# Kernel tuning notes

Measured on AMD Instinct MI355X. Metric: run time of the kernel, lower is better.

## Reference

```python
import jax, jax.numpy as jnp
import numpy as np

NU, NI, NR = 50000, 50000, 5   # users, items, rating levels
D, B, LS, LI = 64, 512, 32, 64 # embed_dim, batch, max social nbrs, max item hist
NEG = -1e9


def setup_inputs() -> dict:
    key = jax.random.key(0)
    ks = iter(jax.random.split(key, 64))
    def lin(din, dout):
        s = 1.0 / np.sqrt(din)
        return (jax.random.uniform(next(ks), (din, dout), minval=-s, maxval=s, dtype=jnp.float32),
                jax.random.uniform(next(ks), (dout,), minval=-s, maxval=s, dtype=jnp.float32))
    inp = {}
    inp['user_w'] = jax.random.normal(next(ks), (NU, D), dtype=jnp.float32) * 0.1
    inp['item_w'] = jax.random.normal(next(ks), (NI, D), dtype=jnp.float32) * 0.1
    inp['rating_w'] = jax.random.normal(next(ks), (NR, D), dtype=jnp.float32) * 0.1
    for name, din, dout in [('i_ln1', 2*D, D), ('i_ln2', D, D), ('i_ln3', 2*D, D),
                            ('i_att1', 2*D, D), ('i_att2', D, D), ('i_att3', D, 1),
                            ('s_ln1', D, D), ('s_ln2', 2*D, D), ('s_ln3', D, D),
                            ('s_att1', 2*D, D), ('s_att2', D, D), ('s_att3', D, 1)]:
        w, b = lin(din, dout)
        inp[name + '_w'] = w
        inp[name + '_b'] = b
    inp['nodes'] = jax.random.randint(next(ks), (B,), 0, NU)
    inp['social_hist'] = jax.random.randint(next(ks), (NU, LS), 0, NU)
    inp['social_mask'] = jax.random.bernoulli(next(ks), 0.5, (NU, LS)).at[:, 0].set(True)
    inp['item_hist'] = jax.random.randint(next(ks), (NU, LI), 0, NI)
    inp['rating_hist'] = jax.random.randint(next(ks), (NU, LI), 0, NR)
    inp['item_mask'] = jax.random.bernoulli(next(ks), 0.5, (NU, LI)).at[:, 0].set(True)
    return inp


def reference(user_w, item_w, rating_w,
              i_ln1_w, i_ln1_b, i_ln2_w, i_ln2_b, i_ln3_w, i_ln3_b,
              i_att1_w, i_att1_b, i_att2_w, i_att2_b, i_att3_w, i_att3_b,
              s_ln1_w, s_ln1_b, s_ln2_w, s_ln2_b, s_ln3_w, s_ln3_b,
              s_att1_w, s_att1_b, s_att2_w, s_att2_b, s_att3_w, s_att3_b,
              nodes, social_hist, social_mask, item_hist, rating_hist, item_mask):
    relu = jax.nn.relu

    def attn(x, w1, b1, w2, b2, w3, b3, mask):
        # x: [..., L, 2D] -> softmax weights over valid neighbors: [..., L]
        h = relu(x @ w1 + b1)
        h = relu(h @ w2 + b2)
        logit = (h @ w3 + b3)[..., 0]
        logit = jnp.where(mask, logit, NEG)
        return jax.nn.softmax(logit, axis=-1)

    def item_final(uids):
        # uids: any shape [...]; returns [..., D]  (Aggre_item.item_final)
        its, rts, m = item_hist[uids], rating_hist[uids], item_mask[uids]
        x = jnp.concatenate([item_w[its], rating_w[rts]], axis=-1)   # [...,LI,2D]
        x = relu(x @ i_ln1_w + i_ln1_b)                              # [...,LI,D]
        u = user_w[uids]                                             # [...,D]
        a_in = jnp.concatenate([x, jnp.broadcast_to(u[..., None, :], x.shape)], axis=-1)
        alpha = attn(a_in, i_att1_w, i_att1_b, i_att2_w, i_att2_b, i_att3_w, i_att3_b, m)
        hI = jnp.einsum('...l,...ld->...d', alpha, x)                # attention-weighted sum
        hI = relu(hI @ i_ln2_w + i_ln2_b)
        return relu(jnp.concatenate([u, hI], axis=-1) @ i_ln3_w + i_ln3_b)

    # item-space factor of query users
    hI_self = item_final(nodes)                                      # [B,D]
    # social aggregation: item_final over each user's social neighbors
    nbrs, nmask = social_hist[nodes], social_mask[nodes]             # [B,LS]
    hI_nb = item_final(nbrs)                                         # [B,LS,D]
    u = user_w[nodes]                                                # [B,D]
    b_in = jnp.concatenate([hI_nb, jnp.broadcast_to(u[:, None, :], hI_nb.shape)], axis=-1)
    beta = attn(b_in, s_att1_w, s_att1_b, s_att2_w, s_att2_b, s_att3_w, s_att3_b, nmask)
    hS = jnp.einsum('bl,bld->bd', beta, hI_nb)
    hS = relu(hS @ s_ln1_w + s_ln1_b)
    f = jnp.concatenate([hI_self, hS], axis=-1)
    f = relu(f @ s_ln2_w + s_ln2_b)
    return relu(f @ s_ln3_w + s_ln3_b)
```

## Files before the change

kernel.cpp:

```cpp
#include <hip/hip_runtime.h>
#include <math.h>


#define NII 50000
#define BB 512
#define LSS 32
#define NT 16896

typedef short short8 __attribute__((ext_vector_type(8)));
typedef float f32x4 __attribute__((ext_vector_type(4)));

static __device__ __forceinline__ bool mread(const void* p, long i, int mode) {
  if (mode == 0) return ((const int*)p)[i] != 0;
  if (mode == 2) return ((const float*)p)[i] != 0.0f;
  return ((const unsigned char*)p)[i] != 0;
}

static __device__ __forceinline__ float wsum(float v) {
#pragma unroll
  for (int s = 1; s < 64; s <<= 1) v += __shfl_xor(v, s);
  return v;
}
static __device__ __forceinline__ float wmax(float v) {
#pragma unroll
  for (int s = 1; s < 64; s <<= 1) v = fmaxf(v, __shfl_xor(v, s));
  return v;
}
static __device__ __forceinline__ float rsum16(float v) {
#pragma unroll
  for (int s = 1; s < 16; s <<= 1) v += __shfl_xor(v, s);
  return v;
}

static __device__ __forceinline__ short bf16rne(float f) {
  unsigned u = __float_as_uint(f);
  u = (u + 0x7FFFu + ((u >> 16) & 1u)) >> 16;
  return (short)u;
}
static __device__ __forceinline__ float bf16tof(short h) {
  return __uint_as_float(((unsigned)(unsigned short)h) << 16);
}

static __device__ __forceinline__ void wave_fence() {
  asm volatile("s_waitcnt lgkmcnt(0)" ::: "memory");
  __builtin_amdgcn_sched_barrier(0);
}

static __device__ __forceinline__ bool inst_uid(int t, const int* nodes,
                                                const int* social_hist,
                                                const void* social_mask,
                                                int mode, long* uid) {
  if (t < BB) {
    *uid = nodes[t];
    return true;
  }
  const int nb = t - BB;
  const int b = nb >> 5, l = nb & 31;
  const long mi = (long)nodes[b] * LSS + l;
  if (!mread(social_mask, mi, mode)) return false;
  *uid = social_hist[mi];
  return true;
}

__global__ void setup_kernel(const unsigned int* __restrict__ sm,
                             int* __restrict__ flag,
                             const float* __restrict__ rating_w,
                             const float* __restrict__ w1,
                             const float* __restrict__ b1,
                             float* __restrict__ RW1g,
                             const float* __restrict__ A1w,
                             const float* __restrict__ A2w,
                             short* __restrict__ B1,
                             short* __restrict__ B2,
                             short* __restrict__ W1hi,
                             short* __restrict__ W1lo) {
  const int tid = threadIdx.x;
  if (blockIdx.x == 0) {
    __shared__ int notInt, notFloat;
    if (tid == 0) { notInt = 0; notFloat = 0; }
    __syncthreads();
    int ni = 0, nf = 0;
    for (int i = tid; i < 4096; i += 256) {
      unsigned int x = sm[i];
      if (x > 1u) ni = 1;
      if (x != 0u && x != 0x3F800000u) nf = 1;
    }
    if (ni) atomicOr(&notInt, 1);
    if (nf) atomicOr(&notFloat, 1);
    __syncthreads();
    if (tid == 0) flag[0] = notInt ? (notFloat ? 1 : 2) : 0;
  } else if (blockIdx.x == 1) {
    for (int t = tid; t < 320; t += 256) {
      const int r = t >> 6, c = t & 63;
      float acc = b1[c];
      for (int k = 0; k < 64; ++k)
        acc = fmaf(rating_w[r * 64 + k], w1[(64 + k) * 64 + c], acc);
      RW1g[r * 64 + c] = acc;
    }
  } else {
    for (int idx = tid; idx < 4096; idx += 256) {
      int e = idx & 7, g = idx >> 3;
      int l = g & 63, q = g >> 6;
      int kb = q >> 2, nb = q & 3;
      int k = kb * 32 + ((l >> 4) & 3) * 8 + e;
      int col = nb * 16 + (l & 15);
      B1[idx] = bf16rne(A1w[k * 64 + col]);
      B2[idx] = bf16rne(A2w[k * 64 + col]);
      float a = w1[k * 64 + col];
      short h = bf16rne(a);
      W1hi[idx] = h;
      W1lo[idx] = bf16rne(a - bf16tof(h));
    }
  }
}

__global__ __launch_bounds__(256, 2)
void mid_kernel(const float* __restrict__ item_w,
                const short* __restrict__ W1hi,
                const short* __restrict__ W1lo,
                short* __restrict__ xbase16,
                const float* __restrict__ user_w,
                const float* __restrict__ A1w, const float* __restrict__ A1b,
                const int* __restrict__ nodes,
                const int* __restrict__ social_hist,
                float* __restrict__ uA1buf) {
  const int tid = threadIdx.x, lane = tid & 63, w = tid >> 6;
  if (blockIdx.x < 512) {
    const int l15 = lane & 15, lg4 = lane >> 4;
    short8 bh[8], bl[8];
#pragma unroll
    for (int q = 0; q < 8; ++q) {
      bh[q] = *(const short8*)(W1hi + (q * 64 + lane) * 8);
      bl[q] = *(const short8*)(W1lo + (q * 64 + lane) * 8);
    }
    const int wid = blockIdx.x * 4 + w;
    for (int tile = wid; tile < 3125; tile += 2048) {
      const long r0 = (long)tile * 16;
      const float* ap = item_w + (r0 + l15) * 64 + lg4 * 8;
      short8 ah[2], al[2];
#pragma unroll
      for (int kb = 0; kb < 2; ++kb) {
        const float4 a = *(const float4*)(ap + kb * 32);
        const float4 b = *(const float4*)(ap + kb * 32 + 4);
        float v[8] = {a.x, a.y, a.z, a.w, b.x, b.y, b.z, b.w};
        short8 hi, lo;
#pragma unroll
        for (int e = 0; e < 8; ++e) {
          short h = bf16rne(v[e]);
          hi[e] = h;
          lo[e] = bf16rne(v[e] - bf16tof(h));
        }
        ah[kb] = hi;
        al[kb] = lo;
      }
#pragma unroll
      for (int nb = 0; nb < 4; ++nb) {
        f32x4 acc = {0.0f, 0.0f, 0.0f, 0.0f};
        acc = __builtin_amdgcn_mfma_f32_16x16x32_bf16(ah[0], bh[0 * 4 + nb], acc, 0, 0, 0);
        acc = __builtin_amdgcn_mfma_f32_16x16x32_bf16(ah[1], bh[1 * 4 + nb], acc, 0, 0, 0);
        acc = __builtin_amdgcn_mfma_f32_16x16x32_bf16(ah[0], bl[0 * 4 + nb], acc, 0, 0, 0);
        acc = __builtin_amdgcn_mfma_f32_16x16x32_bf16(ah[1], bl[1 * 4 + nb], acc, 0, 0, 0);
        acc = __builtin_amdgcn_mfma_f32_16x16x32_bf16(al[0], bh[0 * 4 + nb], acc, 0, 0, 0);
        acc = __builtin_amdgcn_mfma_f32_16x16x32_bf16(al[1], bh[1 * 4 + nb], acc, 0, 0, 0);
#pragma unroll
        for (int r = 0; r < 4; ++r)
          xbase16[(r0 + lg4 * 4 + r) * 64 + nb * 16 + l15] = bf16rne(acc[r]);
      }
    }
  } else {
    const int i0 = (blockIdx.x - 512) * 64;
    __shared__ float sW[64][64], sU[64][64];
    __shared__ float sb[64];
    __shared__ int sUid[64];
    for (int i = tid; i < 4096; i += 256) sW[i >> 6][i & 63] = A1w[4096 + i];
    if (tid < 64) {
      sb[tid] = A1b[tid];
      const int t = i0 + tid;
      int uid;
      if (t < BB) {
        uid = nodes[t];
      } else {
        const int nb = t - BB;
        uid = social_hist[(long)nodes[nb >> 5] * LSS + (nb & 31)];
      }
      sUid[tid] = uid;
    }
    __syncthreads();
    for (int i = tid; i < 4096; i += 256) {
      int r = i >> 6, c = i & 63;
      sU[r][c] = user_w[(long)sUid[r] * 64 + c];
    }
    __syncthreads();
    float acc[16];
#pragma unroll
    for (int r = 0; r < 16; ++r) acc[r] = sb[lane];
    for (int k = 0; k < 64; k += 4) {
      float wv0 = sW[k][lane], wv1 = sW[k + 1][lane];
      float wv2 = sW[k + 2][lane], wv3 = sW[k + 3][lane];
#pragma unroll
      for (int r = 0; r < 16; ++r) {
        const float4 xv = *(const float4*)(&sU[w * 16 + r][k]);
        acc[r] = fmaf(xv.x, wv0, acc[r]);
        acc[r] = fmaf(xv.y, wv1, acc[r]);
        acc[r] = fmaf(xv.z, wv2, acc[r]);
        acc[r] = fmaf(xv.w, wv3, acc[r]);
      }
    }
#pragma unroll
    for (int r = 0; r < 16; ++r)
      uA1buf[(long)(i0 + w * 16 + r) * 64 + lane] = acc[r];
  }
}

__global__ __launch_bounds__(512, 8)
void core_mfma_kernel(const short* __restrict__ xb16,
                      const float* __restrict__ RW1g,
                      const float* __restrict__ uA1buf,
                      const short* __restrict__ Bimg1,
                      const short* __restrict__ Bimg2,
                      const float* __restrict__ A2b,
                      const float* __restrict__ A3w,
                      const int* __restrict__ item_hist,
                      const int* __restrict__ rating_hist,
                      const void* __restrict__ item_mask,
                      const int* __restrict__ flagp,
                      const int* __restrict__ nodes,
                      const int* __restrict__ social_hist,
                      const void* __restrict__ social_mask,
                      float* __restrict__ hvecbuf) {
  __shared__ __align__(16) short sB1[4096], sB2[4096];
  __shared__ __align__(16) char smem[8][3072];
  const int tid = threadIdx.x, lane = tid & 63, w = tid >> 6;

  short* h1w = (short*)(smem[w]);
  float* lgw = (float*)(smem[w] + 2304);
  int* cw = (int*)(smem[w] + 2560);

  ((int4*)sB1)[tid] = ((const int4*)Bimg1)[tid];
  ((int4*)sB2)[tid] = ((const int4*)Bimg2)[tid];
  __syncthreads();

  const int t = blockIdx.x * 8 + w;
  const int mode = flagp[0];
  long uid;
  if (!inst_uid(t, nodes, social_hist, social_mask, mode, &uid))
    return;

  const float a2bv = A2b[lane];
  const float a3v = A3w[lane];
  const int l15 = lane & 15;
  const int lg4 = lane >> 4;

#define B1F(q) (*(const short8*)(sB1 + ((q) * 64 + lane) * 8))
#define B2F(q) (*(const short8*)(sB2 + ((q) * 64 + lane) * 8))

  const long mbase = uid * 64;
  bool mk = mread(item_mask, mbase + lane, mode);
  unsigned long long bal = __ballot(mk);
  const int nact = (int)__popcll(bal);
  int pos = (int)__popcll(bal & ((1ull << lane) - 1ull));
  if (mk) cw[pos] = (item_hist[mbase + lane] << 3) | rating_hist[mbase + lane];
  const float uA1v = uA1buf[(long)t * 64 + lane];
  wave_fence();

  const int ng = (nact + 15) >> 4;
  for (int mc = 0; mc < ng; ++mc) {
    wave_fence();
    int row = mc * 16 + l15;
    if (row >= nact) row = nact - 1;
    const int p = cw[row];
    const long it = p >> 3;
    const int rt = p & 7;
    short8 xa[2];
#pragma unroll
    for (int kb = 0; kb < 2; ++kb) {
      const int koff = kb * 32 + lg4 * 8;
      const short8 xb = *(const short8*)(xb16 + it * 64 + koff);
      const float* rp = RW1g + rt * 64 + koff;
      const float4 c = *(const float4*)rp;
      const float4 d = *(const float4*)(rp + 4);
      short8 f;
      f[0] = bf16rne(fmaxf(bf16tof(xb[0]) + c.x, 0.0f));
      f[1] = bf16rne(fmaxf(bf16tof(xb[1]) + c.y, 0.0f));
      f[2] = bf16rne(fmaxf(bf16tof(xb[2]) + c.z, 0.0f));
      f[3] = bf16rne(fmaxf(bf16tof(xb[3]) + c.w, 0.0f));
      f[4] = bf16rne(fmaxf(bf16tof(xb[4]) + d.x, 0.0f));
      f[5] = bf16rne(fmaxf(bf16tof(xb[5]) + d.y, 0.0f));
      f[6] = bf16rne(fmaxf(bf16tof(xb[6]) + d.z, 0.0f));
      f[7] = bf16rne(fmaxf(bf16tof(xb[7]) + d.w, 0.0f));
      xa[kb] = f;
    }
#pragma unroll
    for (int nb = 0; nb < 4; ++nb) {
      const float ui = __shfl(uA1v, nb * 16 + l15);
      f32x4 acc = {ui, ui, ui, ui};
      acc = __builtin_amdgcn_mfma_f32_16x16x32_bf16(xa[0], B1F(0 * 4 + nb), acc, 0, 0, 0);
      acc = __builtin_amdgcn_mfma_f32_16x16x32_bf16(xa[1], B1F(1 * 4 + nb), acc, 0, 0, 0);
#pragma unroll
      for (int r = 0; r < 4; ++r)
        h1w[(lg4 * 4 + r) * 72 + nb * 16 + l15] = bf16rne(fmaxf(acc[r], 0.0f));
    }
    wave_fence();
    short8 ha[2];
    ha[0] = *(const short8*)(h1w + l15 * 72 + lg4 * 8);
    ha[1] = *(const short8*)(h1w + l15 * 72 + 32 + lg4 * 8);
    float t0 = 0.0f, t1 = 0.0f, t2 = 0.0f, t3 = 0.0f;
#pragma unroll
    for (int nb = 0; nb < 4; ++nb) {
      const float b2 = __shfl(a2bv, nb * 16 + l15);
      f32x4 acc = {b2, b2, b2, b2};
      acc = __builtin_amdgcn_mfma_f32_16x16x32_bf16(ha[0], B2F(0 * 4 + nb), acc, 0, 0, 0);
      acc = __builtin_amdgcn_mfma_f32_16x16x32_bf16(ha[1], B2F(1 * 4 + nb), acc, 0, 0, 0);
      const float a3c = __shfl(a3v, nb * 16 + l15);
      t0 = fmaf(fmaxf(acc[0], 0.0f), a3c, t0);
      t1 = fmaf(fmaxf(acc[1], 0.0f), a3c, t1);
      t2 = fmaf(fmaxf(acc[2], 0.0f), a3c, t2);
      t3 = fmaf(fmaxf(acc[3], 0.0f), a3c, t3);
    }
    t0 = rsum16(t0); t1 = rsum16(t1); t2 = rsum16(t2); t3 = rsum16(t3);
    if (l15 == 0) {
      const int jb = mc * 16 + lg4 * 4;
      lgw[jb + 0] = t0;
      lgw[jb + 1] = t1;
      lgw[jb + 2] = t2;
      lgw[jb + 3] = t3;
    }
  }
  wave_fence();

  const bool valid = (lane < nact);
  float lv = valid ? lgw[lane] : -1e30f;
  float mx = wmax(lv);
  float e = valid ? __expf(lv - mx) : 0.0f;
  float s = wsum(e);
  const float alpha = e / s;

  float h0 = 0.0f, hA = 0.0f, hB = 0.0f, hC = 0.0f;
  int j = 0;
  for (; j + 3 < nact; j += 4) {
    const int p0 = cw[j], p1 = cw[j + 1], p2 = cw[j + 2], p3 = cw[j + 3];
    const float a0 = __shfl(alpha, j), a1 = __shfl(alpha, j + 1);
    const float a2 = __shfl(alpha, j + 2), a3 = __shfl(alpha, j + 3);
    const float x0 = bf16tof(xb16[(long)(p0 >> 3) * 64 + lane]) + RW1g[(p0 & 7) * 64 + lane];
    const float x1 = bf16tof(xb16[(long)(p1 >> 3) * 64 + lane]) + RW1g[(p1 & 7) * 64 + lane];
    const float x2 = bf16tof(xb16[(long)(p2 >> 3) * 64 + lane]) + RW1g[(p2 & 7) * 64 + lane];
    const float x3 = bf16tof(xb16[(long)(p3 >> 3) * 64 + lane]) + RW1g[(p3 & 7) * 64 + lane];
    h0 = fmaf(a0, fmaxf(x0, 0.0f), h0);
    hA = fmaf(a1, fmaxf(x1, 0.0f), hA);
    hB = fmaf(a2, fmaxf(x2, 0.0f), hB);
    hC = fmaf(a3, fmaxf(x3, 0.0f), hC);
  }
  for (; j < nact; ++j) {
    const int p = cw[j];
    const float aj = __shfl(alpha, j);
    const float xv = bf16tof(xb16[(long)(p >> 3) * 64 + lane]) + RW1g[(p & 7) * 64 + lane];
    h0 = fmaf(aj, fmaxf(xv, 0.0f), h0);
  }
  hvecbuf[(long)t * 64 + lane] = (h0 + hA) + (hB + hC);
#undef B1F
#undef B2F
}

__global__ __launch_bounds__(256, 2)
void hI2final_kernel(const float* __restrict__ hvecbuf,
                     const float* __restrict__ user_w,
                     const float* __restrict__ W2w, const float* __restrict__ W2b,
                     const float* __restrict__ W3w, const float* __restrict__ W3b,
                     const int* __restrict__ nodes,
                     const int* __restrict__ social_hist,
                     float* __restrict__ hIbuf) {
  const int tid = threadIdx.x, lane = tid & 63, w = tid >> 6;
  const int i0 = blockIdx.x * 32;
  __shared__ float sW[128][64];
  __shared__ float sX[32][128];
  __shared__ float sb[64];
  __shared__ int sUid[32];
  for (int i = tid; i < 4096; i += 256) sW[i >> 6][i & 63] = W2w[i];
  if (tid < 64) sb[tid] = W2b[tid];
  if (tid < 32) {
    const int t = i0 + tid;
    int uid;
    if (t < BB) {
      uid = nodes[t];
    } else {
      const int nb = t - BB;
      uid = social_hist[(long)nodes[nb >> 5] * LSS + (nb & 31)];
    }
    sUid[tid] = uid;
  }
  __syncthreads();
  for (int i = tid; i < 2048; i += 256) {
    int r = i >> 6, c = i & 63;
    sX[r][64 + c] = hvecbuf[(long)(i0 + r) * 64 + c];
    sX[r][c] = user_w[(long)sUid[r] * 64 + c];
  }
  __syncthreads();

  float acc[8];
  {
    const float bv = sb[lane];
#pragma unroll
    for (int r = 0; r < 8; ++r) acc[r] = bv;
    for (int k = 0; k < 64; k += 4) {
      float wv0 = sW[k][lane], wv1 = sW[k + 1][lane];
      float wv2 = sW[k + 2][lane], wv3 = sW[k + 3][lane];
#pragma unroll
      for (int r = 0; r < 8; ++r) {
        const float4 xv = *(const float4*)(&sX[w * 8 + r][64 + k]);
        acc[r] = fmaf(xv.x, wv0, acc[r]);
        acc[r] = fmaf(xv.y, wv1, acc[r]);
        acc[r] = fmaf(xv.z, wv2, acc[r]);
        acc[r] = fmaf(xv.w, wv3, acc[r]);
      }
    }
#pragma unroll
    for (int r = 0; r < 8; ++r) sX[w * 8 + r][64 + lane] = fmaxf(acc[r], 0.0f);
  }
  __syncthreads();
  for (int i = tid; i < 8192; i += 256) sW[i >> 6][i & 63] = W3w[i];
  if (tid < 64) sb[tid] = W3b[tid];
  __syncthreads();

  {
    const float bv = sb[lane];
#pragma unroll
    for (int r = 0; r < 8; ++r) acc[r] = bv;
    for (int k = 0; k < 128; k += 4) {
      float wv0 = sW[k][lane], wv1 = sW[k + 1][lane];
      float wv2 = sW[k + 2][lane], wv3 = sW[k + 3][lane];
#pragma unroll
      for (int r = 0; r < 8; ++r) {
        const float4 xv = *(const float4*)(&sX[w * 8 + r][k]);
        acc[r] = fmaf(xv.x, wv0, acc[r]);
        acc[r] = fmaf(xv.y, wv1, acc[r]);
        acc[r] = fmaf(xv.z, wv2, acc[r]);
        acc[r] = fmaf(xv.w, wv3, acc[r]);
      }
    }
#pragma unroll
    for (int r = 0; r < 8; ++r)
      hIbuf[(long)(i0 + w * 8 + r) * 64 + lane] = fmaxf(acc[r], 0.0f);
  }
}

__global__ __launch_bounds__(256, 8)
void social_fused_kernel(const float* __restrict__ hIbuf,
                         const float* __restrict__ user_w,
                         const float* __restrict__ S1w,
                         const float* __restrict__ S1b,
                         const float* __restrict__ S2w,
                         const float* __restrict__ S2b,
                         const float* __restrict__ S3w,
                         const float* __restrict__ L1w, const float* __restrict__ L1b,
                         const float* __restrict__ L2w, const float* __restrict__ L2b,
                         const float* __restrict__ L3w, const float* __restrict__ L3b,
                         const int* __restrict__ nodes,
                         const void* __restrict__ social_mask,
                         const int* __restrict__ flagp,
                         float* __restrict__ out) {
  __shared__ __align__(16) short sB1[4096], sB2[4096];
  __shared__ __align__(16) char smem[4][3584];
  const int tid = threadIdx.x, lane = tid & 63, w = tid >> 6;
  short* h1w = (short*)(smem[w]);
  float* lgw = (float*)(smem[w] + 2560);
  int* cw = (int*)(smem[w] + 2816);
  float* vA = (float*)(smem[w] + 3072);
  float* vB = (float*)(smem[w] + 3328);

  for (int i = tid; i < 4096; i += 256) {
    int e = i & 7, g = i >> 3;
    int l = g & 63, q = g >> 6;
    int kb = q >> 2, nb = q & 3;
    int k = kb * 32 + ((l >> 4) & 3) * 8 + e;
    int col = nb * 16 + (l & 15);
    sB1[i] = bf16rne(S1w[k * 64 + col]);
    sB2[i] = bf16rne(S2w[k * 64 + col]);
  }
  __syncthreads();

  const int mode = flagp[0];
  const int l15 = lane & 15;
  const int lg4 = lane >> 4;
  const int b = blockIdx.x * 4 + w;
  const long uid = nodes[b];

  bool m = (lane < LSS) ? mread(social_mask, uid * LSS + lane, mode) : false;
  unsigned long long bal = __ballot(m);
  const int nval = (int)__popcll(bal);
  int pos = (int)__popcll(bal & ((1ull << lane) - 1ull));
  if (m) cw[pos] = lane;

  const float uv = user_w[uid * 64 + lane];
  float uA1v = S1b[lane];
#pragma unroll 8
  for (int k = 0; k < 64; ++k)
    uA1v = fmaf(__shfl(uv, k), S1w[(64 + k) * 64 + lane], uA1v);
  const float a2bv = S2b[lane];
  const float a3v = S3w[lane];
  wave_fence();

  const long hbase = 512L + (long)b * 32;
  const int ng = (nval + 15) >> 4;
  for (int mc = 0; mc < ng; ++mc) {
    wave_fence();
    int row = mc * 16 + l15;
    if (row >= nval) row = nval - 1;
    const long hrow = hbase + cw[row];
    short8 xa[2];
#pragma unroll
    for (int kb = 0; kb < 2; ++kb) {
      const float* xp = hIbuf + hrow * 64 + kb * 32 + lg4 * 8;
      const float4 a = *(const float4*)xp;
      const float4 bb = *(const float4*)(xp + 4);
      short8 f;
      f[0] = bf16rne(a.x);  f[1] = bf16rne(a.y);
      f[2] = bf16rne(a.z);  f[3] = bf16rne(a.w);
      f[4] = bf16rne(bb.x); f[5] = bf16rne(bb.y);
      f[6] = bf16rne(bb.z); f[7] = bf16rne(bb.w);
      xa[kb] = f;
    }
#pragma unroll
    for (int nb = 0; nb < 4; ++nb) {
      const float ui = __shfl(uA1v, nb * 16 + l15);
      f32x4 acc = {ui, ui, ui, ui};
      acc = __builtin_amdgcn_mfma_f32_16x16x32_bf16(
          xa[0], *(const short8*)(sB1 + ((0 * 4 + nb) * 64 + lane) * 8), acc, 0, 0, 0);
      acc = __builtin_amdgcn_mfma_f32_16x16x32_bf16(
          xa[1], *(const short8*)(sB1 + ((1 * 4 + nb) * 64 + lane) * 8), acc, 0, 0, 0);
#pragma unroll
      for (int r = 0; r < 4; ++r)
        h1w[(lg4 * 4 + r) * 80 + nb * 16 + l15] = bf16rne(fmaxf(acc[r], 0.0f));
    }
    wave_fence();
    short8 ha[2];
    ha[0] = *(const short8*)(h1w + l15 * 80 + lg4 * 8);
    ha[1] = *(const short8*)(h1w + l15 * 80 + 32 + lg4 * 8);
    float t0 = 0.0f, t1 = 0.0f, t2 = 0.0f, t3 = 0.0f;
#pragma unroll
    for (int nb = 0; nb < 4; ++nb) {
      const float b2 = __shfl(a2bv, nb * 16 + l15);
      f32x4 acc = {b2, b2, b2, b2};
      acc = __builtin_amdgcn_mfma_f32_16x16x32_bf16(
          ha[0], *(const short8*)(sB2 + ((0 * 4 + nb) * 64 + lane) * 8), acc, 0, 0, 0);
      acc = __builtin_amdgcn_mfma_f32_16x16x32_bf16(
          ha[1], *(const short8*)(sB2 + ((1 * 4 + nb) * 64 + lane) * 8), acc, 0, 0, 0);
      const float a3c = __shfl(a3v, nb * 16 + l15);
      t0 = fmaf(fmaxf(acc[0], 0.0f), a3c, t0);
      t1 = fmaf(fmaxf(acc[1], 0.0f), a3c, t1);
      t2 = fmaf(fmaxf(acc[2], 0.0f), a3c, t2);
      t3 = fmaf(fmaxf(acc[3], 0.0f), a3c, t3);
    }
    t0 = rsum16(t0); t1 = rsum16(t1); t2 = rsum16(t2); t3 = rsum16(t3);
    if (l15 == 0) {
      const int jb = mc * 16 + lg4 * 4;
      lgw[jb + 0] = t0;
      lgw[jb + 1] = t1;
      lgw[jb + 2] = t2;
      lgw[jb + 3] = t3;
    }
  }
  wave_fence();

  const bool valid = (lane < nval);
  float lv = valid ? lgw[lane] : -1e30f;
  float mx = wmax(lv);
  float e = valid ? __expf(lv - mx) : 0.0f;
  float s = wsum(e);
  const float beta = e / s;

  float hs = 0.0f;
  for (int j = 0; j < nval; ++j) {
    const float bj = __shfl(beta, j);
    hs = fmaf(bj, hIbuf[(hbase + cw[j]) * 64 + lane], hs);
  }

  vA[lane] = hs;
  wave_fence();
  float acc = L1b[lane];
#pragma unroll 8
  for (int k = 0; k < 64; ++k) acc = fmaf(vA[k], L1w[k * 64 + lane], acc);
  const float vecB = fmaxf(acc, 0.0f);
  const float selfv = hIbuf[(long)b * 64 + lane];
  wave_fence();
  vA[lane] = selfv;
  vB[lane] = vecB;
  wave_fence();
  acc = L2b[lane];
#pragma unroll 8
  for (int k = 0; k < 64; ++k) acc = fmaf(vA[k], L2w[k * 64 + lane], acc);
#pragma unroll 8
  for (int k = 0; k < 64; ++k) acc = fmaf(vB[k], L2w[(64 + k) * 64 + lane], acc);
  const float fv = fmaxf(acc, 0.0f);
  wave_fence();
  vA[lane] = fv;
  wave_fence();
  acc = L3b[lane];
#pragma unroll 8
  for (int k = 0; k < 64; ++k) acc = fmaf(vA[k], L3w[k * 64 + lane], acc);
  out[(long)b * 64 + lane] = fmaxf(acc, 0.0f);
}

extern "C" void kernel_launch(void* const* d_in, const int* in_sizes, int n_in,
                              void* d_out, int out_size, void* d_ws, size_t ws_size,
                              hipStream_t stream) {
  const float* user_w   = (const float*)d_in[0];
  const float* item_w   = (const float*)d_in[1];
  const float* rating_w = (const float*)d_in[2];
  const float* i_ln1_w  = (const float*)d_in[3];
  const float* i_ln1_b  = (const float*)d_in[4];
  const float* i_ln2_w  = (const float*)d_in[5];
  const float* i_ln2_b  = (const float*)d_in[6];
  const float* i_ln3_w  = (const float*)d_in[7];
  const float* i_ln3_b  = (const float*)d_in[8];
  const float* i_att1_w = (const float*)d_in[9];
  const float* i_att1_b = (const float*)d_in[10];
  const float* i_att2_w = (const float*)d_in[11];
  const float* i_att2_b = (const float*)d_in[12];
  const float* i_att3_w = (const float*)d_in[13];
  const float* i_att3_b = (const float*)d_in[14];
  const float* s_ln1_w  = (const float*)d_in[15];
  const float* s_ln1_b  = (const float*)d_in[16];
  const float* s_ln2_w  = (const float*)d_in[17];
  const float* s_ln2_b  = (const float*)d_in[18];
  const float* s_ln3_w  = (const float*)d_in[19];
  const float* s_ln3_b  = (const float*)d_in[20];
  const float* s_att1_w = (const float*)d_in[21];
  const float* s_att1_b = (const float*)d_in[22];
  const float* s_att2_w = (const float*)d_in[23];
  const float* s_att2_b = (const float*)d_in[24];
  const float* s_att3_w = (const float*)d_in[25];
  const float* s_att3_b = (const float*)d_in[26];
  const int*  nodes       = (const int*)d_in[27];
  const int*  social_hist = (const int*)d_in[28];
  const void* social_mask = d_in[29];
  const int*  item_hist   = (const int*)d_in[30];
  const int*  rating_hist = (const int*)d_in[31];
  const void* item_mask   = d_in[32];

  char* ws = (char*)d_ws;
  int*   flag    = (int*)(ws + 0);
  float* uA1buf  = (float*)(ws + 135680);
  float* hIbuf   = uA1buf;
  float* hvecbuf = (float*)(ws + 4461056);
  short* W1hi    = (short*)(ws + 4461056);
  short* W1lo    = (short*)(ws + 4469248);
  short* xbase16 = (short*)(ws + 8786432);
  float* RW1g    = (float*)(ws + 21586432);
  short* Bimg1   = (short*)(ws + 21587712);
  short* Bimg2   = (short*)(ws + 21595904);

  setup_kernel<<<3, 256, 0, stream>>>(
      (const unsigned int*)social_mask, flag,
      rating_w, i_ln1_w, i_ln1_b, RW1g,
      i_att1_w, i_att2_w, Bimg1, Bimg2, W1hi, W1lo);
  mid_kernel<<<512 + NT / 64, 256, 0, stream>>>(
      item_w, W1hi, W1lo, xbase16,
      user_w, i_att1_w, i_att1_b, nodes, social_hist, uA1buf);
  core_mfma_kernel<<<NT / 8, 512, 0, stream>>>(
      xbase16, RW1g, uA1buf, Bimg1, Bimg2, i_att2_b, i_att3_w,
      item_hist, rating_hist, item_mask, flag,
      nodes, social_hist, social_mask, hvecbuf);
  hI2final_kernel<<<NT / 32, 256, 0, stream>>>(
      hvecbuf, user_w, i_ln2_w, i_ln2_b, i_ln3_w, i_ln3_b,
      nodes, social_hist, hIbuf);
  social_fused_kernel<<<BB / 4, 256, 0, stream>>>(
      hIbuf, user_w, s_att1_w, s_att1_b, s_att2_w, s_att2_b, s_att3_w,
      s_ln1_w, s_ln1_b, s_ln2_w, s_ln2_b, s_ln3_w, s_ln3_b,
      nodes, social_mask, flag, (float*)d_out);
}
```

Before: 107.6 us.

## Software-pipeline item-chunk gathers with double-buffered registers in attention MLP

The loop over 16-row item chunks is unrolled into four fixed stages. The global gather of the next chunk's bf16 item rows is issued before the MFMA work on the current chunk, so memory latency overlaps compute. s_setprio is raised around the MFMA sections to favour this wave's matrix issue. The unrolling assumes at most 64 active items (LI=64), and the extra live registers may reduce occupancy.

```diff
diff --git a/kernel.cpp b/kernel.cpp
--- a/kernel.cpp
+++ b/kernel.cpp
@@ -264,68 +264,94 @@
   wave_fence();
 
   const int ng = (nact + 15) >> 4;
-  for (int mc = 0; mc < ng; ++mc) {
-    wave_fence();
-    int row = mc * 16 + l15;
-    if (row >= nact) row = nact - 1;
-    const int p = cw[row];
-    const long it = p >> 3;
-    const int rt = p & 7;
-    short8 xa[2];
-#pragma unroll
-    for (int kb = 0; kb < 2; ++kb) {
-      const int koff = kb * 32 + lg4 * 8;
-      const short8 xb = *(const short8*)(xb16 + it * 64 + koff);
-      const float* rp = RW1g + rt * 64 + koff;
-      const float4 c = *(const float4*)rp;
-      const float4 d = *(const float4*)(rp + 4);
-      short8 f;
-      f[0] = bf16rne(fmaxf(bf16tof(xb[0]) + c.x, 0.0f));
-      f[1] = bf16rne(fmaxf(bf16tof(xb[1]) + c.y, 0.0f));
-      f[2] = bf16rne(fmaxf(bf16tof(xb[2]) + c.z, 0.0f));
-      f[3] = bf16rne(fmaxf(bf16tof(xb[3]) + c.w, 0.0f));
-      f[4] = bf16rne(fmaxf(bf16tof(xb[4]) + d.x, 0.0f));
-      f[5] = bf16rne(fmaxf(bf16tof(xb[5]) + d.y, 0.0f));
-      f[6] = bf16rne(fmaxf(bf16tof(xb[6]) + d.z, 0.0f));
-      f[7] = bf16rne(fmaxf(bf16tof(xb[7]) + d.w, 0.0f));
-      xa[kb] = f;
-    }
-#pragma unroll
-    for (int nb = 0; nb < 4; ++nb) {
-      const float ui = __shfl(uA1v, nb * 16 + l15);
-      f32x4 acc = {ui, ui, ui, ui};
-      acc = __builtin_amdgcn_mfma_f32_16x16x32_bf16(xa[0], B1F(0 * 4 + nb), acc, 0, 0, 0);
-      acc = __builtin_amdgcn_mfma_f32_16x16x32_bf16(xa[1], B1F(1 * 4 + nb), acc, 0, 0, 0);
-#pragma unroll
-      for (int r = 0; r < 4; ++r)
-        h1w[(lg4 * 4 + r) * 72 + nb * 16 + l15] = bf16rne(fmaxf(acc[r], 0.0f));
-    }
-    wave_fence();
-    short8 ha[2];
-    ha[0] = *(const short8*)(h1w + l15 * 72 + lg4 * 8);
-    ha[1] = *(const short8*)(h1w + l15 * 72 + 32 + lg4 * 8);
-    float t0 = 0.0f, t1 = 0.0f, t2 = 0.0f, t3 = 0.0f;
-#pragma unroll
-    for (int nb = 0; nb < 4; ++nb) {
-      const float b2 = __shfl(a2bv, nb * 16 + l15);
-      f32x4 acc = {b2, b2, b2, b2};
-      acc = __builtin_amdgcn_mfma_f32_16x16x32_bf16(ha[0], B2F(0 * 4 + nb), acc, 0, 0, 0);
-      acc = __builtin_amdgcn_mfma_f32_16x16x32_bf16(ha[1], B2F(1 * 4 + nb), acc, 0, 0, 0);
-      const float a3c = __shfl(a3v, nb * 16 + l15);
-      t0 = fmaf(fmaxf(acc[0], 0.0f), a3c, t0);
-      t1 = fmaf(fmaxf(acc[1], 0.0f), a3c, t1);
-      t2 = fmaf(fmaxf(acc[2], 0.0f), a3c, t2);
-      t3 = fmaf(fmaxf(acc[3], 0.0f), a3c, t3);
-    }
-    t0 = rsum16(t0); t1 = rsum16(t1); t2 = rsum16(t2); t3 = rsum16(t3);
-    if (l15 == 0) {
-      const int jb = mc * 16 + lg4 * 4;
-      lgw[jb + 0] = t0;
-      lgw[jb + 1] = t1;
-      lgw[jb + 2] = t2;
-      lgw[jb + 3] = t3;
-    }
-  }
+  const int pk0 = cw[min(0 * 16 + l15, nact - 1)];
+  const int pk1 = cw[min(1 * 16 + l15, nact - 1)];
+  const int pk2 = cw[min(2 * 16 + l15, nact - 1)];
+  const int pk3 = cw[min(3 * 16 + l15, nact - 1)];
+
+#define ISSUE(PK, G0, G1)                                                   \
+  {                                                                         \
+    const short* xp = xb16 + (long)((PK) >> 3) * 64 + lg4 * 8;              \
+    G0 = *(const short8*)(xp);                                              \
+    G1 = *(const short8*)(xp + 32);                                         \
+  }
+
+#define PROCC(C, PK, G0, G1)                                                \
+  if ((C) < ng) {                                                           \
+    wave_fence();     \
+    short8 xa0, xa1;                                                        \
+    {                                                                       \
+      const float* rp = RW1g + ((PK) & 7) * 64 + lg4 * 8;                   \
+      const float4 c0 = *(const float4*)rp;                                 \
+      const float4 d0 = *(const float4*)(rp + 4);                           \
+      const float4 c1 = *(const float4*)(rp + 32);                          \
+      const float4 d1 = *(const float4*)(rp + 36);                          \
+      xa0[0] = bf16rne(fmaxf(bf16tof(G0[0]) + c0.x, 0.0f));                 \
+      xa0[1] = bf16rne(fmaxf(bf16tof(G0[1]) + c0.y, 0.0f));                 \
+      xa0[2] = bf16rne(fmaxf(bf16tof(G0[2]) + c0.z, 0.0f));                 \
+      xa0[3] = bf16rne(fmaxf(bf16tof(G0[3]) + c0.w, 0.0f));                 \
+      xa0[4] = bf16rne(fmaxf(bf16tof(G0[4]) + d0.x, 0.0f));                 \
+      xa0[5] = bf16rne(fmaxf(bf16tof(G0[5]) + d0.y, 0.0f));                 \
+      xa0[6] = bf16rne(fmaxf(bf16tof(G0[6]) + d0.z, 0.0f));                 \
+      xa0[7] = bf16rne(fmaxf(bf16tof(G0[7]) + d0.w, 0.0f));                 \
+      xa1[0] = bf16rne(fmaxf(bf16tof(G1[0]) + c1.x, 0.0f));                 \
+      xa1[1] = bf16rne(fmaxf(bf16tof(G1[1]) + c1.y, 0.0f));                 \
+      xa1[2] = bf16rne(fmaxf(bf16tof(G1[2]) + c1.z, 0.0f));                 \
+      xa1[3] = bf16rne(fmaxf(bf16tof(G1[3]) + c1.w, 0.0f));                 \
+      xa1[4] = bf16rne(fmaxf(bf16tof(G1[4]) + d1.x, 0.0f));                 \
+      xa1[5] = bf16rne(fmaxf(bf16tof(G1[5]) + d1.y, 0.0f));                 \
+      xa1[6] = bf16rne(fmaxf(bf16tof(G1[6]) + d1.z, 0.0f));                 \
+      xa1[7] = bf16rne(fmaxf(bf16tof(G1[7]) + d1.w, 0.0f));                 \
+    }                                                                       \
+    __builtin_amdgcn_s_setprio(1);                                          \
+    _Pragma("unroll")                                                       \
+    for (int nb = 0; nb < 4; ++nb) {                                        \
+      const float ui = __shfl(uA1v, nb * 16 + l15);                         \
+      f32x4 acc = {ui, ui, ui, ui};                                         \
+      acc = __builtin_amdgcn_mfma_f32_16x16x32_bf16(xa0, B1F(nb), acc, 0, 0, 0);      \
+      acc = __builtin_amdgcn_mfma_f32_16x16x32_bf16(xa1, B1F(4 + nb), acc, 0, 0, 0);  \
+      _Pragma("unroll")                                                     \
+      for (int r = 0; r < 4; ++r)                                           \
+        h1w[(lg4 * 4 + r) * 72 + nb * 16 + l15] = bf16rne(fmaxf(acc[r], 0.0f)); \
+    }                                                                       \
+    __builtin_amdgcn_s_setprio(0);                                          \
+    wave_fence();                                                           \
+    {                                                                       \
+      const short8 ha0 = *(const short8*)(h1w + l15 * 72 + lg4 * 8);        \
+      const short8 ha1 = *(const short8*)(h1w + l15 * 72 + 32 + lg4 * 8);   \
+      float t0 = 0.0f, t1 = 0.0f, t2 = 0.0f, t3 = 0.0f;                     \
+      __builtin_amdgcn_s_setprio(1);                                        \
+      _Pragma("unroll")                                                     \
+      for (int nb = 0; nb < 4; ++nb) {                                      \
+        const float b2 = __shfl(a2bv, nb * 16 + l15);                       \
+        f32x4 acc = {b2, b2, b2, b2};                                       \
+        acc = __builtin_amdgcn_mfma_f32_16x16x32_bf16(ha0, B2F(nb), acc, 0, 0, 0);     \
+        acc = __builtin_amdgcn_mfma_f32_16x16x32_bf16(ha1, B2F(4 + nb), acc, 0, 0, 0); \
+        const float a3c = __shfl(a3v, nb * 16 + l15);                       \
+        t0 = fmaf(fmaxf(acc[0], 0.0f), a3c, t0);                            \
+        t1 = fmaf(fmaxf(acc[1], 0.0f), a3c, t1);                            \
+        t2 = fmaf(fmaxf(acc[2], 0.0f), a3c, t2);                            \
+        t3 = fmaf(fmaxf(acc[3], 0.0f), a3c, t3);                            \
+      }                                                                     \
+      __builtin_amdgcn_s_setprio(0);                                        \
+      t0 = rsum16(t0); t1 = rsum16(t1); t2 = rsum16(t2); t3 = rsum16(t3);   \
+      if (l15 == 0) {                                                       \
+        const int jb = (C) * 16 + lg4 * 4;                                  \
+        lgw[jb + 0] = t0; lgw[jb + 1] = t1;                                 \
+        lgw[jb + 2] = t2; lgw[jb + 3] = t3;                                 \
+      }                                                                     \
+    }                                                                       \
+  }
+
+  short8 ga0, ga1, gb0, gb1;
+  ISSUE(pk0, ga0, ga1);
+  if (1 < ng) ISSUE(pk1, gb0, gb1);
+  PROCC(0, pk0, ga0, ga1);
+  if (2 < ng) ISSUE(pk2, ga0, ga1);
+  PROCC(1, pk1, gb0, gb1);
+  if (3 < ng) ISSUE(pk3, gb0, gb1);
+  PROCC(2, pk2, ga0, ga1);
+  PROCC(3, pk3, gb0, gb1);
   wave_fence();
 
   const bool valid = (lane < nact);
@@ -359,6 +385,8 @@
   hvecbuf[(long)t * 64 + lane] = (h0 + hA) + (hB + hC);
 #undef B1F
 #undef B2F
+#undef ISSUE
+#undef PROCC
 }
 
 __global__ __launch_bounds__(256, 2)
```

After: 109.0 us. Within noise of the previous version (+1.3%).
